# Kernel tuning notes

Measured on AMD Instinct MI355X. Metric: run time of the kernel, lower is better.

The kernel has to match this reference:

```python
import jax, jax.numpy as jnp
from jax import lax
import numpy as np

BATCH, SEQ, VOCAB, EMB, UNIT = 256, 512, 50000, 128, 512


def setup_inputs() -> dict:
    key = jax.random.key(0)
    ks = jax.random.split(key, 8)
    s = 0.05  # keep tanh out of saturation
    return {
        "tokens": jax.random.randint(ks[0], (BATCH, SEQ), 0, VOCAB, dtype=jnp.int32),
        "emb": jax.random.normal(ks[1], (VOCAB, EMB), jnp.float32) * s,
        "Wx0": jax.random.normal(ks[2], (EMB, UNIT), jnp.float32) * s,
        "Wh0": jax.random.normal(ks[3], (UNIT, UNIT), jnp.float32) * s,
        "b0": jnp.zeros((UNIT,), jnp.float32),
        "Wx1": jax.random.normal(ks[4], (UNIT, UNIT), jnp.float32) * s,
        "Wh1": jax.random.normal(ks[5], (UNIT, UNIT), jnp.float32) * s,
        "b1": jnp.zeros((UNIT,), jnp.float32),
        "fc_w": jax.random.normal(ks[6], (UNIT, 1), jnp.float32) * s,
        "fc_b": jnp.zeros((1,), jnp.float32),
    }


def reference(tokens, emb, Wx0, Wh0, b0, Wx1, Wh1, b1, fc_w, fc_b):
    # Embedding lookup: [B, T, E]
    x = emb[tokens]
    B = tokens.shape[0]
    U = Wh0.shape[0]

    def step(carry, xt):
        h0, h1, h2 = carry
        # SimpleRNNCell: h' = tanh(x @ Wx + h @ Wh + b); dropout inactive (training=None)
        h0n = jnp.tanh(xt @ Wx0 + h0 @ Wh0 + b0)
        # NOTE: original code reuses rnncell1 weights for both layer 1 and layer 2 (bug kept)
        h1n = jnp.tanh(h0n @ Wx1 + h1 @ Wh1 + b1)
        h2n = jnp.tanh(h1n @ Wx1 + h2 @ Wh1 + b1)
        return (h0n, h1n, h2n), None

    init = tuple(jnp.zeros((B, U), x.dtype) for _ in range(3))
    (h0, h1, h2), _ = lax.scan(step, init, jnp.swapaxes(x, 0, 1))  # scan over time [T, B, E]
    logits = h2 @ fc_w + fc_b  # [B, 1]
    return jax.nn.sigmoid(logits)
```

## Files before the change

### kernel.cpp

```cpp
#include <hip/hip_runtime.h>


#define BATCH 256
#define SEQ   512
#define EMBD  128
#define UNIT  512

typedef _Float16 half8 __attribute__((ext_vector_type(8)));
typedef _Float16 half4 __attribute__((ext_vector_type(4)));
typedef float    f32x4 __attribute__((ext_vector_type(4)));
typedef unsigned int uint4v __attribute__((ext_vector_type(4)));
typedef int      int4v __attribute__((ext_vector_type(4)));

#define FLAGS_BYTES 4096
#define HBUF_OFF    4096
#define HBUF_ELEMS  (3*8*4*32*512)
#define HBUF_BYTES  (HBUF_ELEMS*2)
#define PWX0_OFF    (HBUF_OFF + HBUF_BYTES)
#define PWH0_OFF    (PWX0_OFF + EMBD*UNIT*2)
#define PWX1_OFF    (PWH0_OFF + UNIT*UNIT*2)
#define PWH1_OFF    (PWX1_OFF + UNIT*UNIT*2)

__device__ __forceinline__ void sc_st_int(int* p, int v) {
    asm volatile("global_store_dword %0, %1, off sc0 sc1" :: "v"(p), "v"(v) : "memory");
}

__device__ __forceinline__ void sc_ld_q3(const int* p0, const int* p1, const int* p2,
                                         int4v& a, int4v& b, int4v& c) {
    asm volatile(
        "global_load_dwordx4 %0, %3, off sc0 sc1\n\t"
        "global_load_dwordx4 %1, %4, off sc0 sc1\n\t"
        "global_load_dwordx4 %2, %5, off sc0 sc1\n\t"
        "s_waitcnt vmcnt(0)"
        : "=&v"(a), "=&v"(b), "=&v"(c)
        : "v"(p0), "v"(p1), "v"(p2)
        : "memory");
}

__device__ __forceinline__ void sc_load14(
    const uint4v* a0, const uint4v* a1, const uint4v* a2,
    const uint4v* a3, const uint4v* a4, const uint4v* a5,
    const uint4v* b0, const uint4v* b1, const uint4v* b2, const uint4v* b3,
    const uint4v* b4, const uint4v* b5, const uint4v* b6, const uint4v* b7,
    uint4v& s0, uint4v& s1, uint4v& s2, uint4v& s3, uint4v& s4, uint4v& s5,
    uint4v& r0, uint4v& r1, uint4v& r2, uint4v& r3,
    uint4v& r4, uint4v& r5, uint4v& r6, uint4v& r7)
{
    asm volatile(
        "global_load_dwordx4 %0, %14, off sc0 sc1\n\t"
        "global_load_dwordx4 %1, %15, off sc0 sc1\n\t"
        "global_load_dwordx4 %2, %16, off sc0 sc1\n\t"
        "global_load_dwordx4 %3, %17, off sc0 sc1\n\t"
        "global_load_dwordx4 %4, %18, off sc0 sc1\n\t"
        "global_load_dwordx4 %5, %19, off sc0 sc1\n\t"
        "global_load_dwordx4 %6, %20, off sc0 sc1\n\t"
        "global_load_dwordx4 %7, %21, off sc0 sc1\n\t"
        "global_load_dwordx4 %8, %22, off sc0 sc1\n\t"
        "global_load_dwordx4 %9, %23, off sc0 sc1\n\t"
        "global_load_dwordx4 %10, %24, off sc0 sc1\n\t"
        "global_load_dwordx4 %11, %25, off sc0 sc1\n\t"
        "global_load_dwordx4 %12, %26, off sc0 sc1\n\t"
        "global_load_dwordx4 %13, %27, off sc0 sc1\n\t"
        "s_waitcnt vmcnt(0)"
        : "=&v"(s0), "=&v"(s1), "=&v"(s2), "=&v"(s3), "=&v"(s4), "=&v"(s5),
          "=&v"(r0), "=&v"(r1), "=&v"(r2), "=&v"(r3),
          "=&v"(r4), "=&v"(r5), "=&v"(r6), "=&v"(r7)
        : "v"(a0), "v"(a1), "v"(a2), "v"(a3), "v"(a4), "v"(a5),
          "v"(b0), "v"(b1), "v"(b2), "v"(b3), "v"(b4), "v"(b5), "v"(b6), "v"(b7)
        : "memory");
}

__device__ __forceinline__ void sc_load6(
    const uint4v* p0, const uint4v* p1, const uint4v* p2,
    const uint4v* p3, const uint4v* p4, const uint4v* p5,
    uint4v& r0, uint4v& r1, uint4v& r2, uint4v& r3, uint4v& r4, uint4v& r5)
{
    asm volatile(
        "global_load_dwordx4 %0, %6, off sc0 sc1\n\t"
        "global_load_dwordx4 %1, %7, off sc0 sc1\n\t"
        "global_load_dwordx4 %2, %8, off sc0 sc1\n\t"
        "global_load_dwordx4 %3, %9, off sc0 sc1\n\t"
        "global_load_dwordx4 %4, %10, off sc0 sc1\n\t"
        "global_load_dwordx4 %5, %11, off sc0 sc1\n\t"
        "s_waitcnt vmcnt(0)"
        : "=&v"(r0), "=&v"(r1), "=&v"(r2), "=&v"(r3), "=&v"(r4), "=&v"(r5)
        : "v"(p0), "v"(p1), "v"(p2), "v"(p3), "v"(p4), "v"(p5)
        : "memory");
}

__device__ __forceinline__ void sc_store2(uint4v* p0, uint4v v0, uint4v* p1, uint4v v1) {
    asm volatile(
        "global_store_dwordx4 %0, %2, off sc0 sc1\n\t"
        "global_store_dwordx4 %1, %3, off sc0 sc1\n\t"
        "s_waitcnt vmcnt(0)"
        :: "v"(p0), "v"(p1), "v"(v0), "v"(v1)
        : "memory");
}

__global__ void zero_ws_kernel(uint4v* __restrict__ p, int n16) {
    int i = blockIdx.x * 256 + threadIdx.x;
    uint4v z = {0u, 0u, 0u, 0u};
    if (i < n16) p[i] = z;
}

__global__ void pack_w_kernel(const float* __restrict__ src, _Float16* __restrict__ dst,
                              int K, int N) {
    int idx = blockIdx.x * 256 + threadIdx.x;
    if (idx >= K * N) return;
    int j    = idx & 7;
    int lane = (idx >> 3) & 63;
    int rest = idx >> 9;
    int KT   = K >> 5;
    int kt   = rest % KT;
    int nt   = rest / KT;
    int k = kt*32 + (lane >> 4)*8 + j;
    int n = nt*16 + (lane & 15);
    dst[idx] = (_Float16)src[k * N + n];
}

__global__ __launch_bounds__(256, 1)
void rnn_main_kernel(const int*   __restrict__ tokens,
                     const float* __restrict__ emb,
                     const float* __restrict__ b0,
                     const float* __restrict__ b1,
                     char* ws)
{
    const int bid   = blockIdx.x;
    const int layer = bid >> 5;
    const int mg    = (bid >> 2) & 7;
    const int ns    = bid & 3;
    const int tid   = threadIdx.x;
    const int wv    = tid >> 6;
    const int lane  = tid & 63;
    const int q     = lane >> 4;
    const int c16   = lane & 15;

    int* flags = (int*)ws;
    int* qOwn  = flags + (layer*8 + mg)*32;
    int* qUp   = flags + ((layer > 0 ? layer-1 : layer)*8 + mg)*32;
    int* qDn   = flags + ((layer < 2 ? layer+1 : layer)*8 + mg)*32;

    _Float16* hbuf = (_Float16*)(ws + HBUF_OFF);
    const _Float16* pWh = (const _Float16*)(ws + (layer == 0 ? PWH0_OFF : PWH1_OFF));
    const _Float16* pWx = (const _Float16*)(ws + (layer == 0 ? PWX0_OFF : PWX1_OFF));
    const float* bias = (layer == 0) ? b0 : b1;

    const int c0  = ns*128 + wv*32;
    const int nt0 = c0 >> 4;

    __shared__ _Float16 Ah [32][512];
    __shared__ _Float16 Ain[32][512];
    __shared__ _Float16 Bounce[32][128];

    {
        uint4v z = {0u,0u,0u,0u};
#pragma unroll
        for (int i = 0; i < 8; ++i) ((uint4v*)Ah)[i*256 + tid] = z;
    }

    half8 whf[16][2];
    half8 wxf[16][2];
#pragma unroll
    for (int kt = 0; kt < 16; ++kt)
#pragma unroll
        for (int n = 0; n < 2; ++n)
            whf[kt][n] = *(const half8*)&pWh[(((nt0 + n)*16 + kt)*64 + lane) * 8];
    if (layer == 0) {
#pragma unroll
        for (int kt = 0; kt < 4; ++kt)
#pragma unroll
            for (int n = 0; n < 2; ++n)
                wxf[kt][n] = *(const half8*)&pWx[(((nt0 + n)*4 + kt)*64 + lane) * 8];
    } else {
#pragma unroll
        for (int kt = 0; kt < 16; ++kt)
#pragma unroll
            for (int n = 0; n < 2; ++n)
                wxf[kt][n] = *(const half8*)&pWx[(((nt0 + n)*16 + kt)*64 + lane) * 8];
    }

    const float bv0 = bias[c0 + c16];
    const float bv1 = bias[c0 + 16 + c16];

    const int m0       = mg * 32;
    const int slotBase = (layer*8 + mg) * 4;

    const int sA = (ns == 0) ? 1 : 0;
    const int sB = (ns <= 1) ? 2 : 1;
    const int sC = (ns <= 2) ? 3 : 2;

    for (int t = 0; t < SEQ; ++t) {
        if (tid == 0) {
            for (;;) {
                int4v o, u, d;
                sc_ld_q3(qOwn, qUp, qDn, o, u, d);
                int mo = o[0] < o[1] ? o[0] : o[1];
                mo = mo < o[2] ? mo : o[2]; mo = mo < o[3] ? mo : o[3];
                int mu = u[0] < u[1] ? u[0] : u[1];
                mu = mu < u[2] ? mu : u[2]; mu = mu < u[3] ? mu : u[3];
                int md = d[0] < d[1] ? d[0] : d[1];
                md = md < d[2] ? md : d[2]; md = md < d[3] ? md : d[3];
                bool ok = (mo >= t);
                if (layer > 0)            ok = ok && (mu >= t + 1);
                if (layer < 2 && t >= 4)  ok = ok && (md >= t - 3);
                if (ok) break;
                __builtin_amdgcn_s_sleep(1);
            }
        }
        __syncthreads();

        const uint4v* tp = (const uint4v*)(hbuf + (slotBase + ((t + 3) & 3)) * 16384);
        const int j0 = 2*tid, j1 = j0 + 1;
        const int r0i = j0 >> 4, cl0 = j0 & 15;
        const int r1i = j1 >> 4, cl1 = j1 & 15;
        const int ccA0 = sA*16 + cl0, ccA1 = sA*16 + cl1;
        const int ccB0 = sB*16 + cl0, ccB1 = sB*16 + cl1;
        const int ccC0 = sC*16 + cl0, ccC1 = sC*16 + cl1;

        f32x4 acc00 = {0,0,0,0}, acc01 = {0,0,0,0}, acc10 = {0,0,0,0}, acc11 = {0,0,0,0};

        if (layer > 0) {
            const uint4v* sb = (const uint4v*)
                (hbuf + (((layer-1)*8 + mg)*4 + (t & 3)) * 16384);
            uint4v s0,s1,s2,s3,s4,s5, rr0,rr1,rr2,rr3,rr4,rr5,rr6,rr7;
            sc_load14(tp + r0i*64 + ccA0, tp + r1i*64 + ccA1,
                      tp + r0i*64 + ccB0, tp + r1i*64 + ccB1,
                      tp + r0i*64 + ccC0, tp + r1i*64 + ccC1,
                      sb +        tid, sb +  256 + tid, sb +  512 + tid, sb +  768 + tid,
                      sb + 1024 + tid, sb + 1280 + tid, sb + 1536 + tid, sb + 1792 + tid,
                      s0, s1, s2, s3, s4, s5,
                      rr0, rr1, rr2, rr3, rr4, rr5, rr6, rr7);
            *(uint4v*)&Ah[r0i][((ccA0 + r0i) & 63) * 8] = s0;
            *(uint4v*)&Ah[r1i][((ccA1 + r1i) & 63) * 8] = s1;
            *(uint4v*)&Ah[r0i][((ccB0 + r0i) & 63) * 8] = s2;
            *(uint4v*)&Ah[r1i][((ccB1 + r1i) & 63) * 8] = s3;
            *(uint4v*)&Ah[r0i][((ccC0 + r0i) & 63) * 8] = s4;
            *(uint4v*)&Ah[r1i][((ccC1 + r1i) & 63) * 8] = s5;
#pragma unroll
            for (int i = 0; i < 8; ++i) {
                uint4v v = (i==0)?rr0:(i==1)?rr1:(i==2)?rr2:(i==3)?rr3:
                           (i==4)?rr4:(i==5)?rr5:(i==6)?rr6:rr7;
                int ci = i*256 + tid;
                int r  = ci >> 6;
                int cc = ci & 63;
                *(uint4v*)&Ain[r][((cc + r) & 63) * 8] = v;
            }
            __syncthreads();

#pragma unroll
            for (int kt = 0; kt < 16; ++kt) {
                half8 a0 = *(const half8*)&Ah[c16]     [((kt*4 + q + c16)      & 63) * 8];
                half8 a1 = *(const half8*)&Ah[16 + c16][((kt*4 + q + 16 + c16) & 63) * 8];
                acc00 = __builtin_amdgcn_mfma_f32_16x16x32_f16(a0, whf[kt][0], acc00, 0, 0, 0);
                acc01 = __builtin_amdgcn_mfma_f32_16x16x32_f16(a0, whf[kt][1], acc01, 0, 0, 0);
                acc10 = __builtin_amdgcn_mfma_f32_16x16x32_f16(a1, whf[kt][0], acc10, 0, 0, 0);
                acc11 = __builtin_amdgcn_mfma_f32_16x16x32_f16(a1, whf[kt][1], acc11, 0, 0, 0);
            }
#pragma unroll
            for (int kt = 0; kt < 16; ++kt) {
                half8 a0 = *(const half8*)&Ain[c16]     [((kt*4 + q + c16)      & 63) * 8];
                half8 a1 = *(const half8*)&Ain[16 + c16][((kt*4 + q + 16 + c16) & 63) * 8];
                acc00 = __builtin_amdgcn_mfma_f32_16x16x32_f16(a0, wxf[kt][0], acc00, 0, 0, 0);
                acc01 = __builtin_amdgcn_mfma_f32_16x16x32_f16(a0, wxf[kt][1], acc01, 0, 0, 0);
                acc10 = __builtin_amdgcn_mfma_f32_16x16x32_f16(a1, wxf[kt][0], acc10, 0, 0, 0);
                acc11 = __builtin_amdgcn_mfma_f32_16x16x32_f16(a1, wxf[kt][1], acc11, 0, 0, 0);
            }
        } else {
            uint4v s0, s1, s2, s3, s4, s5;
            sc_load6(tp + r0i*64 + ccA0, tp + r1i*64 + ccA1,
                     tp + r0i*64 + ccB0, tp + r1i*64 + ccB1,
                     tp + r0i*64 + ccC0, tp + r1i*64 + ccC1,
                     s0, s1, s2, s3, s4, s5);
            *(uint4v*)&Ah[r0i][((ccA0 + r0i) & 63) * 8] = s0;
            *(uint4v*)&Ah[r1i][((ccA1 + r1i) & 63) * 8] = s1;
            *(uint4v*)&Ah[r0i][((ccB0 + r0i) & 63) * 8] = s2;
            *(uint4v*)&Ah[r1i][((ccB1 + r1i) & 63) * 8] = s3;
            *(uint4v*)&Ah[r0i][((ccC0 + r0i) & 63) * 8] = s4;
            *(uint4v*)&Ah[r1i][((ccC1 + r1i) & 63) * 8] = s5;
#pragma unroll
            for (int i = 0; i < 4; ++i) {
                int idx = i*256 + tid;
                int r   = idx >> 5;
                int qq  = idx & 31;
                int tok = tokens[(m0 + r)*SEQ + t];
                float4 f = *((const float4*)(emb + (long)tok * EMBD) + qq);
                half4 h = { (_Float16)f.x, (_Float16)f.y, (_Float16)f.z, (_Float16)f.w };
                *(half4*)&Ain[r][((((qq >> 1) + r) & 63) * 8) + (qq & 1) * 4] = h;
            }
            __syncthreads();

#pragma unroll
            for (int kt = 0; kt < 16; ++kt) {
                half8 a0 = *(const half8*)&Ah[c16]     [((kt*4 + q + c16)      & 63) * 8];
                half8 a1 = *(const half8*)&Ah[16 + c16][((kt*4 + q + 16 + c16) & 63) * 8];
                acc00 = __builtin_amdgcn_mfma_f32_16x16x32_f16(a0, whf[kt][0], acc00, 0, 0, 0);
                acc01 = __builtin_amdgcn_mfma_f32_16x16x32_f16(a0, whf[kt][1], acc01, 0, 0, 0);
                acc10 = __builtin_amdgcn_mfma_f32_16x16x32_f16(a1, whf[kt][0], acc10, 0, 0, 0);
                acc11 = __builtin_amdgcn_mfma_f32_16x16x32_f16(a1, whf[kt][1], acc11, 0, 0, 0);
            }
#pragma unroll
            for (int kt = 0; kt < 4; ++kt) {
                half8 a0 = *(const half8*)&Ain[c16]     [((kt*4 + q + c16)      & 63) * 8];
                half8 a1 = *(const half8*)&Ain[16 + c16][((kt*4 + q + 16 + c16) & 63) * 8];
                acc00 = __builtin_amdgcn_mfma_f32_16x16x32_f16(a0, wxf[kt][0], acc00, 0, 0, 0);
                acc01 = __builtin_amdgcn_mfma_f32_16x16x32_f16(a0, wxf[kt][1], acc01, 0, 0, 0);
                acc10 = __builtin_amdgcn_mfma_f32_16x16x32_f16(a1, wxf[kt][0], acc10, 0, 0, 0);
                acc11 = __builtin_amdgcn_mfma_f32_16x16x32_f16(a1, wxf[kt][1], acc11, 0, 0, 0);
            }
        }

        _Float16 hv[16];
#pragma unroll
        for (int r = 0; r < 4; ++r) {
            int row0 = q*4 + r, row1 = 16 + row0;
            float z, e; _Float16 v;
            z = acc00[r] + bv0; e = __expf(2.0f*z); v = (_Float16)(1.0f - 2.0f/(e + 1.0f));
            hv[r*4+0] = v; Bounce[row0][wv*32 + c16]      = v;
            z = acc01[r] + bv1; e = __expf(2.0f*z); v = (_Float16)(1.0f - 2.0f/(e + 1.0f));
            hv[r*4+1] = v; Bounce[row0][wv*32 + 16 + c16] = v;
            z = acc10[r] + bv0; e = __expf(2.0f*z); v = (_Float16)(1.0f - 2.0f/(e + 1.0f));
            hv[r*4+2] = v; Bounce[row1][wv*32 + c16]      = v;
            z = acc11[r] + bv1; e = __expf(2.0f*z); v = (_Float16)(1.0f - 2.0f/(e + 1.0f));
            hv[r*4+3] = v; Bounce[row1][wv*32 + 16 + c16] = v;
        }
        __syncthreads();

        {
            int g0 = c0 + c16, g1 = c0 + 16 + c16;
#pragma unroll
            for (int r = 0; r < 4; ++r) {
                int row0 = q*4 + r, row1 = 16 + row0;
                Ah[row0][(((g0 >> 3) + row0) & 63)*8 + (g0 & 7)] = hv[r*4+0];
                Ah[row0][(((g1 >> 3) + row0) & 63)*8 + (g1 & 7)] = hv[r*4+1];
                Ah[row1][(((g0 >> 3) + row1) & 63)*8 + (g0 & 7)] = hv[r*4+2];
                Ah[row1][(((g1 >> 3) + row1) & 63)*8 + (g1 & 7)] = hv[r*4+3];
            }
            _Float16* tc = hbuf + (slotBase + (t & 3)) * 16384;
            uint4v v0 = ((const uint4v*)Bounce)[j0];
            uint4v v1 = ((const uint4v*)Bounce)[j1];
            uint4v* d0 = (uint4v*)(tc + (j0 >> 4)*512 + ns*128) + (j0 & 15);
            uint4v* d1 = (uint4v*)(tc + (j1 >> 4)*512 + ns*128) + (j1 & 15);
            sc_store2(d0, v0, d1, v1);
        }
        __syncthreads();
        if (tid == 0) sc_st_int(qOwn + ns, t + 1);
    }
}

__global__ void fc_kernel(const char* __restrict__ ws,
                          const float* __restrict__ fc_w,
                          const float* __restrict__ fc_b,
                          float* __restrict__ out)
{
    int row  = blockIdx.x;
    int lane = threadIdx.x;
    int m = row >> 5, lr = row & 31;
    const _Float16* h2 = (const _Float16*)(ws + HBUF_OFF)
                         + (((2*8 + m)*4 + 3) * 16384)
                         + lr * UNIT;
    half8 hv = *(const half8*)&h2[lane * 8];
    const float* w = fc_w + lane * 8;
    float s = 0.0f;
#pragma unroll
    for (int j = 0; j < 8; ++j) s += (float)hv[j] * w[j];
#pragma unroll
    for (int off = 32; off > 0; off >>= 1) s += __shfl_down(s, off);
    if (lane == 0) {
        float logit = s + fc_b[0];
        out[row] = 1.0f / (1.0f + __expf(-logit));
    }
}

extern "C" void kernel_launch(void* const* d_in, const int* in_sizes, int n_in,
                              void* d_out, int out_size, void* d_ws, size_t ws_size,
                              hipStream_t stream)
{
    const int*   tokens = (const int*)  d_in[0];
    const float* emb    = (const float*)d_in[1];
    const float* Wx0    = (const float*)d_in[2];
    const float* Wh0    = (const float*)d_in[3];
    const float* b0     = (const float*)d_in[4];
    const float* Wx1    = (const float*)d_in[5];
    const float* Wh1    = (const float*)d_in[6];
    const float* b1     = (const float*)d_in[7];
    const float* fcw    = (const float*)d_in[8];
    const float* fcb    = (const float*)d_in[9];
    char*  ws  = (char*)d_ws;
    float* out = (float*)d_out;

    int n16 = (FLAGS_BYTES + HBUF_BYTES) / 16;
    zero_ws_kernel<<<(n16 + 255)/256, 256, 0, stream>>>((uint4v*)ws, n16);

    pack_w_kernel<<<(EMBD*UNIT + 255)/256, 256, 0, stream>>>(Wx0, (_Float16*)(ws + PWX0_OFF), EMBD, UNIT);
    pack_w_kernel<<<(UNIT*UNIT + 255)/256, 256, 0, stream>>>(Wh0, (_Float16*)(ws + PWH0_OFF), UNIT, UNIT);
    pack_w_kernel<<<(UNIT*UNIT + 255)/256, 256, 0, stream>>>(Wx1, (_Float16*)(ws + PWX1_OFF), UNIT, UNIT);
    pack_w_kernel<<<(UNIT*UNIT + 255)/256, 256, 0, stream>>>(Wh1, (_Float16*)(ws + PWH1_OFF), UNIT, UNIT);

    rnn_main_kernel<<<96, 256, 0, stream>>>(tokens, emb, b0, b1, ws);

    fc_kernel<<<256, 64, 0, stream>>>((const char*)ws, fcw, fcb, out);
}
```

Measured before the change: 2.632 ms.

## Prefetch lower-layer input via LDS DMA and store hidden state pre-swizzled

When the upstream layer is already a step ahead, the next step's input activations are fetched with global_load_lds DMA straight into LDS instead of through registers. The hidden-state buffer in global memory is now written in the swizzled LDS layout, so Ah refresh uses vector copies from Bounce and the fc kernel un-rotates its weight index. The store wait is moved after the LDS writes. This adds a shared flag, an extra condition on the spin-wait, and depends on the async DMA finishing before the barrier, with different layouts for the DMA and register paths.

```diff
diff --git a/kernel.cpp b/kernel.cpp
--- a/kernel.cpp
+++ b/kernel.cpp
@@ -88,13 +88,22 @@
         : "memory");
 }
 
-__device__ __forceinline__ void sc_store2(uint4v* p0, uint4v v0, uint4v* p1, uint4v v1) {
+__device__ __forceinline__ void sc_store2_nw(uint4v* p0, uint4v v0, uint4v* p1, uint4v v1) {
     asm volatile(
         "global_store_dwordx4 %0, %2, off sc0 sc1\n\t"
-        "global_store_dwordx4 %1, %3, off sc0 sc1\n\t"
-        "s_waitcnt vmcnt(0)"
+        "global_store_dwordx4 %1, %3, off sc0 sc1"
         :: "v"(p0), "v"(p1), "v"(v0), "v"(v1)
         : "memory");
+}
+__device__ __forceinline__ void vm_drain() {
+    asm volatile("s_waitcnt vmcnt(0)" ::: "memory");
+}
+
+__device__ __forceinline__ void lds_dma16(const void* g, void* l) {
+    __builtin_amdgcn_global_load_lds(
+        (const __attribute__((address_space(1))) void*)g,
+        (__attribute__((address_space(3))) void*)l,
+        16, 0, 17);
 }
 
 __global__ void zero_ws_kernel(uint4v* __restrict__ p, int n16) {
@@ -151,12 +160,14 @@
     __shared__ _Float16 Ah [32][512];
     __shared__ _Float16 Ain[32][512];
     __shared__ _Float16 Bounce[32][128];
+    __shared__ int      PFn[1];
 
     {
         uint4v z = {0u,0u,0u,0u};
 #pragma unroll
         for (int i = 0; i < 8; ++i) ((uint4v*)Ah)[i*256 + tid] = z;
     }
+    if (tid == 0) PFn[0] = 0;
 
     half8 whf[16][2];
     half8 wxf[16][2];
@@ -188,6 +199,17 @@
     const int sA = (ns == 0) ? 1 : 0;
     const int sB = (ns <= 1) ? 2 : 1;
     const int sC = (ns <= 2) ? 3 : 2;
+
+    const int j0 = 2*tid, j1 = j0 + 1;
+    const int r0i = j0 >> 4, cl0 = j0 & 15;
+    const int r1i = j1 >> 4, cl1 = j1 & 15;
+    const int pA0 = (sA*16 + cl0 + r0i) & 63, pA1 = (sA*16 + cl1 + r1i) & 63;
+    const int pB0 = (sB*16 + cl0 + r0i) & 63, pB1 = (sB*16 + cl1 + r1i) & 63;
+    const int pC0 = (sC*16 + cl0 + r0i) & 63, pC1 = (sC*16 + cl1 + r1i) & 63;
+    const int pO0 = (ns*16 + cl0 + r0i) & 63, pO1 = (ns*16 + cl1 + r1i) & 63;
+
+    __syncthreads();
+    bool pfCur = false;
 
     for (int t = 0; t < SEQ; ++t) {
         if (tid == 0) {
@@ -203,59 +225,90 @@
                 bool ok = (mo >= t);
                 if (layer > 0)            ok = ok && (mu >= t + 1);
                 if (layer < 2 && t >= 4)  ok = ok && (md >= t - 3);
-                if (ok) break;
+                if (ok) {
+                    PFn[0] = (layer > 0 && mu >= t + 2) ? 1 : 0;
+                    break;
+                }
                 __builtin_amdgcn_s_sleep(1);
             }
         }
         __syncthreads();
+        const bool pfNext = (PFn[0] != 0);
 
         const uint4v* tp = (const uint4v*)(hbuf + (slotBase + ((t + 3) & 3)) * 16384);
-        const int j0 = 2*tid, j1 = j0 + 1;
-        const int r0i = j0 >> 4, cl0 = j0 & 15;
-        const int r1i = j1 >> 4, cl1 = j1 & 15;
-        const int ccA0 = sA*16 + cl0, ccA1 = sA*16 + cl1;
-        const int ccB0 = sB*16 + cl0, ccB1 = sB*16 + cl1;
-        const int ccC0 = sC*16 + cl0, ccC1 = sC*16 + cl1;
-
-        f32x4 acc00 = {0,0,0,0}, acc01 = {0,0,0,0}, acc10 = {0,0,0,0}, acc11 = {0,0,0,0};
-
-        if (layer > 0) {
-            const uint4v* sb = (const uint4v*)
-                (hbuf + (((layer-1)*8 + mg)*4 + (t & 3)) * 16384);
+        const _Float16* sb = hbuf + (((layer > 0 ? layer-1 : 0)*8 + mg)*4 + (t & 3)) * 16384;
+
+        if (layer > 0 && pfCur) {
+#pragma unroll
+            for (int i = 0; i < 8; ++i) {
+                int row = wv*8 + i;
+                lds_dma16(sb + row*512 + lane*8, &Ain[row][0]);
+            }
+        }
+
+        if (layer > 0 && !pfCur) {
+            const uint4v* sbq = (const uint4v*)sb;
             uint4v s0,s1,s2,s3,s4,s5, rr0,rr1,rr2,rr3,rr4,rr5,rr6,rr7;
-            sc_load14(tp + r0i*64 + ccA0, tp + r1i*64 + ccA1,
-                      tp + r0i*64 + ccB0, tp + r1i*64 + ccB1,
-                      tp + r0i*64 + ccC0, tp + r1i*64 + ccC1,
-                      sb +        tid, sb +  256 + tid, sb +  512 + tid, sb +  768 + tid,
-                      sb + 1024 + tid, sb + 1280 + tid, sb + 1536 + tid, sb + 1792 + tid,
+            sc_load14(tp + r0i*64 + pA0, tp + r1i*64 + pA1,
+                      tp + r0i*64 + pB0, tp + r1i*64 + pB1,
+                      tp + r0i*64 + pC0, tp + r1i*64 + pC1,
+                      sbq +        tid, sbq +  256 + tid, sbq +  512 + tid, sbq +  768 + tid,
+                      sbq + 1024 + tid, sbq + 1280 + tid, sbq + 1536 + tid, sbq + 1792 + tid,
                       s0, s1, s2, s3, s4, s5,
                       rr0, rr1, rr2, rr3, rr4, rr5, rr6, rr7);
-            *(uint4v*)&Ah[r0i][((ccA0 + r0i) & 63) * 8] = s0;
-            *(uint4v*)&Ah[r1i][((ccA1 + r1i) & 63) * 8] = s1;
-            *(uint4v*)&Ah[r0i][((ccB0 + r0i) & 63) * 8] = s2;
-            *(uint4v*)&Ah[r1i][((ccB1 + r1i) & 63) * 8] = s3;
-            *(uint4v*)&Ah[r0i][((ccC0 + r0i) & 63) * 8] = s4;
-            *(uint4v*)&Ah[r1i][((ccC1 + r1i) & 63) * 8] = s5;
+            *(uint4v*)&Ah[r0i][pA0 * 8] = s0;
+            *(uint4v*)&Ah[r1i][pA1 * 8] = s1;
+            *(uint4v*)&Ah[r0i][pB0 * 8] = s2;
+            *(uint4v*)&Ah[r1i][pB1 * 8] = s3;
+            *(uint4v*)&Ah[r0i][pC0 * 8] = s4;
+            *(uint4v*)&Ah[r1i][pC1 * 8] = s5;
 #pragma unroll
             for (int i = 0; i < 8; ++i) {
                 uint4v v = (i==0)?rr0:(i==1)?rr1:(i==2)?rr2:(i==3)?rr3:
                            (i==4)?rr4:(i==5)?rr5:(i==6)?rr6:rr7;
                 int ci = i*256 + tid;
-                int r  = ci >> 6;
-                int cc = ci & 63;
-                *(uint4v*)&Ain[r][((cc + r) & 63) * 8] = v;
-            }
-            __syncthreads();
-
-#pragma unroll
-            for (int kt = 0; kt < 16; ++kt) {
-                half8 a0 = *(const half8*)&Ah[c16]     [((kt*4 + q + c16)      & 63) * 8];
-                half8 a1 = *(const half8*)&Ah[16 + c16][((kt*4 + q + 16 + c16) & 63) * 8];
-                acc00 = __builtin_amdgcn_mfma_f32_16x16x32_f16(a0, whf[kt][0], acc00, 0, 0, 0);
-                acc01 = __builtin_amdgcn_mfma_f32_16x16x32_f16(a0, whf[kt][1], acc01, 0, 0, 0);
-                acc10 = __builtin_amdgcn_mfma_f32_16x16x32_f16(a1, whf[kt][0], acc10, 0, 0, 0);
-                acc11 = __builtin_amdgcn_mfma_f32_16x16x32_f16(a1, whf[kt][1], acc11, 0, 0, 0);
-            }
+                *(uint4v*)&Ain[ci >> 6][(ci & 63) * 8] = v;
+            }
+        } else {
+            uint4v s0, s1, s2, s3, s4, s5;
+            sc_load6(tp + r0i*64 + pA0, tp + r1i*64 + pA1,
+                     tp + r0i*64 + pB0, tp + r1i*64 + pB1,
+                     tp + r0i*64 + pC0, tp + r1i*64 + pC1,
+                     s0, s1, s2, s3, s4, s5);
+            *(uint4v*)&Ah[r0i][pA0 * 8] = s0;
+            *(uint4v*)&Ah[r1i][pA1 * 8] = s1;
+            *(uint4v*)&Ah[r0i][pB0 * 8] = s2;
+            *(uint4v*)&Ah[r1i][pB1 * 8] = s3;
+            *(uint4v*)&Ah[r0i][pC0 * 8] = s4;
+            *(uint4v*)&Ah[r1i][pC1 * 8] = s5;
+            if (layer == 0) {
+#pragma unroll
+                for (int i = 0; i < 4; ++i) {
+                    int idx = i*256 + tid;
+                    int r   = idx >> 5;
+                    int qq  = idx & 31;
+                    int tok = tokens[(m0 + r)*SEQ + t];
+                    float4 f = *((const float4*)(emb + (long)tok * EMBD) + qq);
+                    half4 h = { (_Float16)f.x, (_Float16)f.y, (_Float16)f.z, (_Float16)f.w };
+                    int pc = ((qq >> 1) + r) & 63;
+                    *(half4*)&Ain[r][pc*8 + (qq & 1)*4] = h;
+                }
+            }
+        }
+        __syncthreads();
+
+        f32x4 acc00 = {0,0,0,0}, acc01 = {0,0,0,0}, acc10 = {0,0,0,0}, acc11 = {0,0,0,0};
+
+#pragma unroll
+        for (int kt = 0; kt < 16; ++kt) {
+            half8 a0 = *(const half8*)&Ah[c16]     [((kt*4 + q + c16)      & 63) * 8];
+            half8 a1 = *(const half8*)&Ah[16 + c16][((kt*4 + q + 16 + c16) & 63) * 8];
+            acc00 = __builtin_amdgcn_mfma_f32_16x16x32_f16(a0, whf[kt][0], acc00, 0, 0, 0);
+            acc01 = __builtin_amdgcn_mfma_f32_16x16x32_f16(a0, whf[kt][1], acc01, 0, 0, 0);
+            acc10 = __builtin_amdgcn_mfma_f32_16x16x32_f16(a1, whf[kt][0], acc10, 0, 0, 0);
+            acc11 = __builtin_amdgcn_mfma_f32_16x16x32_f16(a1, whf[kt][1], acc11, 0, 0, 0);
+        }
+        if (layer > 0) {
 #pragma unroll
             for (int kt = 0; kt < 16; ++kt) {
                 half8 a0 = *(const half8*)&Ain[c16]     [((kt*4 + q + c16)      & 63) * 8];
@@ -266,38 +319,6 @@
                 acc11 = __builtin_amdgcn_mfma_f32_16x16x32_f16(a1, wxf[kt][1], acc11, 0, 0, 0);
             }
         } else {
-            uint4v s0, s1, s2, s3, s4, s5;
-            sc_load6(tp + r0i*64 + ccA0, tp + r1i*64 + ccA1,
-                     tp + r0i*64 + ccB0, tp + r1i*64 + ccB1,
-                     tp + r0i*64 + ccC0, tp + r1i*64 + ccC1,
-                     s0, s1, s2, s3, s4, s5);
-            *(uint4v*)&Ah[r0i][((ccA0 + r0i) & 63) * 8] = s0;
-            *(uint4v*)&Ah[r1i][((ccA1 + r1i) & 63) * 8] = s1;
-            *(uint4v*)&Ah[r0i][((ccB0 + r0i) & 63) * 8] = s2;
-            *(uint4v*)&Ah[r1i][((ccB1 + r1i) & 63) * 8] = s3;
-            *(uint4v*)&Ah[r0i][((ccC0 + r0i) & 63) * 8] = s4;
-            *(uint4v*)&Ah[r1i][((ccC1 + r1i) & 63) * 8] = s5;
-#pragma unroll
-            for (int i = 0; i < 4; ++i) {
-                int idx = i*256 + tid;
-                int r   = idx >> 5;
-                int qq  = idx & 31;
-                int tok = tokens[(m0 + r)*SEQ + t];
-                float4 f = *((const float4*)(emb + (long)tok * EMBD) + qq);
-                half4 h = { (_Float16)f.x, (_Float16)f.y, (_Float16)f.z, (_Float16)f.w };
-                *(half4*)&Ain[r][((((qq >> 1) + r) & 63) * 8) + (qq & 1) * 4] = h;
-            }
-            __syncthreads();
-
-#pragma unroll
-            for (int kt = 0; kt < 16; ++kt) {
-                half8 a0 = *(const half8*)&Ah[c16]     [((kt*4 + q + c16)      & 63) * 8];
-                half8 a1 = *(const half8*)&Ah[16 + c16][((kt*4 + q + 16 + c16) & 63) * 8];
-                acc00 = __builtin_amdgcn_mfma_f32_16x16x32_f16(a0, whf[kt][0], acc00, 0, 0, 0);
-                acc01 = __builtin_amdgcn_mfma_f32_16x16x32_f16(a0, whf[kt][1], acc01, 0, 0, 0);
-                acc10 = __builtin_amdgcn_mfma_f32_16x16x32_f16(a1, whf[kt][0], acc10, 0, 0, 0);
-                acc11 = __builtin_amdgcn_mfma_f32_16x16x32_f16(a1, whf[kt][1], acc11, 0, 0, 0);
-            }
 #pragma unroll
             for (int kt = 0; kt < 4; ++kt) {
                 half8 a0 = *(const half8*)&Ain[c16]     [((kt*4 + q + c16)      & 63) * 8];
@@ -309,41 +330,34 @@
             }
         }
 
-        _Float16 hv[16];
 #pragma unroll
         for (int r = 0; r < 4; ++r) {
             int row0 = q*4 + r, row1 = 16 + row0;
-            float z, e; _Float16 v;
-            z = acc00[r] + bv0; e = __expf(2.0f*z); v = (_Float16)(1.0f - 2.0f/(e + 1.0f));
-            hv[r*4+0] = v; Bounce[row0][wv*32 + c16]      = v;
-            z = acc01[r] + bv1; e = __expf(2.0f*z); v = (_Float16)(1.0f - 2.0f/(e + 1.0f));
-            hv[r*4+1] = v; Bounce[row0][wv*32 + 16 + c16] = v;
-            z = acc10[r] + bv0; e = __expf(2.0f*z); v = (_Float16)(1.0f - 2.0f/(e + 1.0f));
-            hv[r*4+2] = v; Bounce[row1][wv*32 + c16]      = v;
-            z = acc11[r] + bv1; e = __expf(2.0f*z); v = (_Float16)(1.0f - 2.0f/(e + 1.0f));
-            hv[r*4+3] = v; Bounce[row1][wv*32 + 16 + c16] = v;
+            float z, e;
+            z = acc00[r] + bv0; e = __expf(2.0f*z);
+            Bounce[row0][wv*32 + c16]      = (_Float16)(1.0f - 2.0f/(e + 1.0f));
+            z = acc01[r] + bv1; e = __expf(2.0f*z);
+            Bounce[row0][wv*32 + 16 + c16] = (_Float16)(1.0f - 2.0f/(e + 1.0f));
+            z = acc10[r] + bv0; e = __expf(2.0f*z);
+            Bounce[row1][wv*32 + c16]      = (_Float16)(1.0f - 2.0f/(e + 1.0f));
+            z = acc11[r] + bv1; e = __expf(2.0f*z);
+            Bounce[row1][wv*32 + 16 + c16] = (_Float16)(1.0f - 2.0f/(e + 1.0f));
         }
         __syncthreads();
 
         {
-            int g0 = c0 + c16, g1 = c0 + 16 + c16;
-#pragma unroll
-            for (int r = 0; r < 4; ++r) {
-                int row0 = q*4 + r, row1 = 16 + row0;
-                Ah[row0][(((g0 >> 3) + row0) & 63)*8 + (g0 & 7)] = hv[r*4+0];
-                Ah[row0][(((g1 >> 3) + row0) & 63)*8 + (g1 & 7)] = hv[r*4+1];
-                Ah[row1][(((g0 >> 3) + row1) & 63)*8 + (g0 & 7)] = hv[r*4+2];
-                Ah[row1][(((g1 >> 3) + row1) & 63)*8 + (g1 & 7)] = hv[r*4+3];
-            }
+            uint4v v0 = *(const uint4v*)&Bounce[r0i][cl0 * 8];
+            uint4v v1 = *(const uint4v*)&Bounce[r1i][cl1 * 8];
             _Float16* tc = hbuf + (slotBase + (t & 3)) * 16384;
-            uint4v v0 = ((const uint4v*)Bounce)[j0];
-            uint4v v1 = ((const uint4v*)Bounce)[j1];
-            uint4v* d0 = (uint4v*)(tc + (j0 >> 4)*512 + ns*128) + (j0 & 15);
-            uint4v* d1 = (uint4v*)(tc + (j1 >> 4)*512 + ns*128) + (j1 & 15);
-            sc_store2(d0, v0, d1, v1);
-        }
+            sc_store2_nw((uint4v*)(tc + r0i*512) + pO0, v0,
+                         (uint4v*)(tc + r1i*512) + pO1, v1);
+            *(uint4v*)&Ah[r0i][pO0 * 8] = v0;
+            *(uint4v*)&Ah[r1i][pO1 * 8] = v1;
+        }
+        vm_drain();
         __syncthreads();
         if (tid == 0) sc_st_int(qOwn + ns, t + 1);
+        pfCur = pfNext;
     }
 }
 
@@ -359,7 +373,8 @@
                          + (((2*8 + m)*4 + 3) * 16384)
                          + lr * UNIT;
     half8 hv = *(const half8*)&h2[lane * 8];
-    const float* w = fc_w + lane * 8;
+    int c = (lane - lr) & 63;
+    const float* w = fc_w + c * 8;
     float s = 0.0f;
 #pragma unroll
     for (int j = 0; j < 8; ++j) s += (float)hv[j] * w[j];
```

New measurement: 3.597 ms. +36.7%, slower.
